# Kernel tuning notes

Measured on AMD Instinct MI355X. Metric: run time of the kernel, lower is better.

Reference implementation:

```python
import jax, jax.numpy as jnp
import numpy as np

HIDDEN = 2048
HEADS = 16
HEAD_DIM = HIDDEN // HEADS
BATCH = 2
SEQ = 2048


def setup_inputs() -> dict:
    key = jax.random.key(0)
    ks = jax.random.split(key, 9)
    s = 0.02
    return {
        "x": jax.random.normal(ks[0], (BATCH, SEQ, HIDDEN), dtype=jnp.float32),
        "Wq": jax.random.normal(ks[1], (HIDDEN, HIDDEN), dtype=jnp.float32) * s,
        "bq": jax.random.normal(ks[2], (HIDDEN,), dtype=jnp.float32) * s,
        "Wk": jax.random.normal(ks[3], (HIDDEN, HIDDEN), dtype=jnp.float32) * s,
        "bk": jax.random.normal(ks[4], (HIDDEN,), dtype=jnp.float32) * s,
        "Wv": jax.random.normal(ks[5], (HIDDEN, HIDDEN), dtype=jnp.float32) * s,
        "bv": jax.random.normal(ks[6], (HIDDEN,), dtype=jnp.float32) * s,
        "Wo": jax.random.normal(ks[7], (HIDDEN, HIDDEN), dtype=jnp.float32) * s,
        "bo": jax.random.normal(ks[8], (HIDDEN,), dtype=jnp.float32) * s,
    }


def reference(x, Wq, bq, Wk, bk, Wv, bv, Wo, bo):
    B, S, H = x.shape
    # Linear layers: y = x @ W.T + b (torch nn.Linear convention, W:[out,in])
    q = x @ Wq.T + bq
    k = x @ Wk.T + bk
    v = x @ Wv.T + bv
    # [B, S, H] -> [B, nH, S, hd]
    def split_heads(t):
        return t.reshape(B, S, HEADS, HEAD_DIM).transpose(0, 2, 1, 3)
    q, k, v = split_heads(q), split_heads(k), split_heads(v)
    scale = 1.0 / (HEAD_DIM ** 0.5)
    # NOTE: original module applies NO causal mask despite its name; be faithful.
    scores = jnp.einsum('bhqd,bhkd->bhqk', q, k) * scale
    probs = jax.nn.softmax(scores, axis=-1)
    attn = jnp.einsum('bhqk,bhkd->bhqd', probs, v)
    attn = attn.transpose(0, 2, 1, 3).reshape(B, S, H)
    return attn @ Wo.T + bo
```

## Files before the change

### kernel.cpp

```cpp
#include <hip/hip_runtime.h>
#include <hip/hip_bf16.h>
#include <stdint.h>

typedef __bf16 bf16_t;
typedef __attribute__((ext_vector_type(8))) __bf16 bf16x8;
typedef __attribute__((ext_vector_type(4))) float floatx4;
typedef __attribute__((ext_vector_type(16))) float f32x16;

typedef __attribute__((address_space(1))) const unsigned int gu32_t;
typedef __attribute__((address_space(3))) unsigned int lu32_t;

#define SL2E 0.12753102149f

__device__ __forceinline__ void async16(const void* g, void* l) {
    __builtin_amdgcn_global_load_lds((gu32_t*)g, (lu32_t*)l, 16, 0, 0);
}

__device__ __forceinline__ uint32_t pack2(float lo, float hi) {
    union { bf16_t h[2]; uint32_t u; } cv;
    cv.h[0] = (bf16_t)lo; cv.h[1] = (bf16_t)hi;
    return cv.u;
}

__global__ __launch_bounds__(256) void cvt_all(const float* __restrict__ x,
                                               const float* __restrict__ w0,
                                               const float* __restrict__ w1,
                                               const float* __restrict__ w2,
                                               const float* __restrict__ w3,
                                               bf16_t* __restrict__ out) {
    int b = blockIdx.x;
    const float* in;
    if (b < 4096) {
        in = x + (size_t)b * 2048;
    } else {
        int t = b - 4096;
        const float* wsrc[4] = {w0, w1, w2, w3};
        in = wsrc[t >> 11] + (size_t)(t & 2047) * 2048;
    }
    bf16_t* o = out + (size_t)b * 2048;
    int i = threadIdx.x * 8;
    float4 a = *(const float4*)(in + i);
    float4 c = *(const float4*)(in + i + 4);
    bf16x8 v;
    v[0] = (bf16_t)a.x; v[1] = (bf16_t)a.y; v[2] = (bf16_t)a.z; v[3] = (bf16_t)a.w;
    v[4] = (bf16_t)c.x; v[5] = (bf16_t)c.y; v[6] = (bf16_t)c.z; v[7] = (bf16_t)c.w;
    *(bf16x8*)(o + i) = v;
}

__global__ __launch_bounds__(256) void gemm_qkv(const bf16_t* __restrict__ xb,
                                                const bf16_t* __restrict__ wqk,
                                                const bf16_t* __restrict__ wv,
                                                const float* __restrict__ bq,
                                                const float* __restrict__ bk,
                                                const float* __restrict__ bv,
                                                bf16_t* __restrict__ QKb,
                                                bf16_t* __restrict__ Vtb) {
    __shared__ bf16_t As[128 * 64];
    __shared__ bf16_t Bs[128 * 64];
    const int tid = threadIdx.x;
    const int wave = tid >> 6, lane = tid & 63;
    const int quad = lane >> 4, l16 = lane & 15;
    const int wm = (wave >> 1) * 64, wn = (wave & 1) * 64;

    const int bid = blockIdx.x;
    const bool vmode = bid >= 1024;
    int tm, tn;
    const bf16_t *A, *B;
    bf16_t* Cb;
    if (!vmode) { tm = (bid & 31) * 128; tn = (bid >> 5) * 128; A = xb; B = wqk; Cb = QKb; }
    else { int vb = bid - 1024; tm = (vb & 15) * 128; tn = (vb >> 4) * 128; A = wv; B = xb; Cb = Vtb; }
    const int K = 2048, ldc = 4096;

    floatx4 acc[4][4];
#pragma unroll
    for (int i = 0; i < 4; ++i)
#pragma unroll
        for (int j = 0; j < 4; ++j) acc[i][j] = floatx4{0.f, 0.f, 0.f, 0.f};

    const bf16_t* Abase = A + (size_t)tm * K;
    const bf16_t* Bbase = B + (size_t)tn * K;
    const int sw = l16 & 7;

    for (int kk = 0; kk < K; kk += 64) {
#pragma unroll
        for (int it = 0; it < 4; ++it) {
            int chunk = it * 256 + tid;
            int r = chunk >> 3, c = chunk & 7;
            int c2 = c ^ (r & 7);
            async16(Abase + r * K + kk + c2 * 8, As + (it * 256 + wave * 64) * 8);
            async16(Bbase + r * K + kk + c2 * 8, Bs + (it * 256 + wave * 64) * 8);
        }
        __syncthreads();
#pragma unroll
        for (int ks = 0; ks < 2; ++ks) {
            bf16x8 af[4], bf[4];
#pragma unroll
            for (int mt = 0; mt < 4; ++mt)
                af[mt] = *(const bf16x8*)(As + (wm + mt * 16 + l16) * 64 +
                                          ((ks * 4 + quad) ^ sw) * 8);
#pragma unroll
            for (int nt = 0; nt < 4; ++nt)
                bf[nt] = *(const bf16x8*)(Bs + (wn + nt * 16 + l16) * 64 +
                                          ((ks * 4 + quad) ^ sw) * 8);
#pragma unroll
            for (int mt = 0; mt < 4; ++mt)
#pragma unroll
                for (int nt = 0; nt < 4; ++nt)
                    acc[mt][nt] = __builtin_amdgcn_mfma_f32_16x16x32_bf16(af[mt], bf[nt],
                                                                          acc[mt][nt], 0, 0, 0);
        }
        __syncthreads();
    }
#pragma unroll
    for (int mt = 0; mt < 4; ++mt)
#pragma unroll
        for (int nt = 0; nt < 4; ++nt)
#pragma unroll
            for (int r = 0; r < 4; ++r) {
                int row = tm + wm + mt * 16 + quad * 4 + r;
                int col = tn + wn + nt * 16 + l16;
                float v;
                if (vmode) v = acc[mt][nt][r] + bv[row];
                else if (col < 2048) v = (acc[mt][nt][r] + bq[col]) * SL2E;
                else v = acc[mt][nt][r] + bk[col - 2048];
                Cb[(size_t)row * ldc + col] = (bf16_t)v;
            }
}

__global__ __launch_bounds__(256) void gemm_out(const bf16_t* __restrict__ A,
                                                const bf16_t* __restrict__ B,
                                                const float* __restrict__ bias,
                                                float* __restrict__ Cf,
                                                int K, int ldc) {
    __shared__ bf16_t As[128 * 64];
    __shared__ bf16_t Bs[128 * 64];
    const int tid = threadIdx.x;
    const int wave = tid >> 6, lane = tid & 63;
    const int quad = lane >> 4, l16 = lane & 15;
    const int wm = (wave >> 1) * 64, wn = (wave & 1) * 64;
    const int tm = blockIdx.x * 128, tn = blockIdx.y * 128;

    floatx4 acc[4][4];
#pragma unroll
    for (int i = 0; i < 4; ++i)
#pragma unroll
        for (int j = 0; j < 4; ++j) acc[i][j] = floatx4{0.f, 0.f, 0.f, 0.f};

    const bf16_t* Abase = A + (size_t)tm * K;
    const bf16_t* Bbase = B + (size_t)tn * K;
    const int sw = l16 & 7;

    for (int kk = 0; kk < K; kk += 64) {
#pragma unroll
        for (int it = 0; it < 4; ++it) {
            int chunk = it * 256 + tid;
            int r = chunk >> 3, c = chunk & 7;
            int c2 = c ^ (r & 7);
            async16(Abase + r * K + kk + c2 * 8, As + (it * 256 + wave * 64) * 8);
            async16(Bbase + r * K + kk + c2 * 8, Bs + (it * 256 + wave * 64) * 8);
        }
        __syncthreads();
#pragma unroll
        for (int ks = 0; ks < 2; ++ks) {
            bf16x8 af[4], bf[4];
#pragma unroll
            for (int mt = 0; mt < 4; ++mt)
                af[mt] = *(const bf16x8*)(As + (wm + mt * 16 + l16) * 64 +
                                          ((ks * 4 + quad) ^ sw) * 8);
#pragma unroll
            for (int nt = 0; nt < 4; ++nt)
                bf[nt] = *(const bf16x8*)(Bs + (wn + nt * 16 + l16) * 64 +
                                          ((ks * 4 + quad) ^ sw) * 8);
#pragma unroll
            for (int mt = 0; mt < 4; ++mt)
#pragma unroll
                for (int nt = 0; nt < 4; ++nt)
                    acc[mt][nt] = __builtin_amdgcn_mfma_f32_16x16x32_bf16(af[mt], bf[nt],
                                                                          acc[mt][nt], 0, 0, 0);
        }
        __syncthreads();
    }
#pragma unroll
    for (int mt = 0; mt < 4; ++mt)
#pragma unroll
        for (int nt = 0; nt < 4; ++nt)
#pragma unroll
            for (int r = 0; r < 4; ++r) {
                int row = tm + wm + mt * 16 + quad * 4 + r;
                int col = tn + wn + nt * 16 + l16;
                Cf[(size_t)row * ldc + col] = acc[mt][nt][r] + bias[col];
            }
}

#define FA_BUF (64 * 128 + 128 * 64)
__global__ __launch_bounds__(256, 2) void flash_attn(const bf16_t* __restrict__ Qp,
                                                     const bf16_t* __restrict__ Kp,
                                                     const bf16_t* __restrict__ Vt,
                                                     bf16_t* __restrict__ O) {
    __shared__ bf16_t smem[2 * FA_BUF];
    const int tid = threadIdx.x;
    const int wv = tid >> 6, lane = tid & 63;
    const int hi = lane >> 5, l32 = lane & 31;
    const int wq = wv >> 1, wk = wv & 1;
    const int LD = 4096, T = 4096, S = 2048, HO = 2048;

    const int gid = blockIdx.x;
    const int kq = gid >> 3;
    const int qt = kq & 15;
    const int grp = (gid & 7) + 8 * (kq >> 4);
    const int hd = grp & 15, bt = grp >> 4;

    const int qrow0 = bt * S + qt * 128;
    const int krow0 = bt * S;
    const int hoff = hd * 128;
    const int sw7 = l32 & 7;

    bf16x8 qf[2][8];
#pragma unroll
    for (int g = 0; g < 2; ++g) {
        const bf16_t* qptr = Qp + (size_t)(qrow0 + wq * 64 + g * 32 + l32) * LD + hoff + hi * 8;
#pragma unroll
        for (int ks = 0; ks < 8; ++ks) qf[g][ks] = *(const bf16x8*)(qptr + ks * 16);
    }

    float l_i[2] = {0.f, 0.f};
    f32x16 Oacc[2][4];
#pragma unroll
    for (int g = 0; g < 2; ++g)
#pragma unroll
        for (int dt = 0; dt < 4; ++dt)
#pragma unroll
            for (int r = 0; r < 16; ++r) Oacc[g][dt][r] = 0.f;

    auto stage = [&](int kt, int b) {
        int kb = krow0 + kt * 64;
        bf16_t* Ks = smem + b * FA_BUF;
        bf16_t* Vts = Ks + 64 * 128;
#pragma unroll
        for (int it = 0; it < 4; ++it) {
            int chunk = it * 256 + tid;
            int r = chunk >> 4, c = chunk & 15;
            int c2 = c ^ (r & 7);
            async16(Kp + (size_t)(kb + r) * LD + hoff + c2 * 8, Ks + chunk * 8);
        }
#pragma unroll
        for (int it = 0; it < 4; ++it) {
            int chunk = it * 256 + tid;
            int r = chunk >> 3, c = chunk & 7;
            int c2 = c ^ (r & 7);
            async16(Vt + (size_t)(hoff + r) * T + kb + c2 * 8, Vts + chunk * 8);
        }
    };

    stage(0, 0);
    for (int kt = 0; kt < 32; ++kt) {
        const int cur = kt & 1;
        __syncthreads();
        if (kt + 1 < 32) stage(kt + 1, cur ^ 1);

        const bf16_t* Ks = smem + cur * FA_BUF;
        const bf16_t* Vts = Ks + 64 * 128;

        uint32_t pk[2][8];
#pragma unroll
        for (int g = 0; g < 2; ++g) {
            f32x16 sf;
#pragma unroll
            for (int r = 0; r < 16; ++r) sf[r] = 0.f;
#pragma unroll
            for (int ks = 0; ks < 8; ++ks) {
                bf16x8 a = *(const bf16x8*)(Ks + (wk * 32 + l32) * 128 +
                                            ((2 * ks + hi) ^ sw7) * 8);
                sf = __builtin_amdgcn_mfma_f32_32x32x16_bf16(a, qf[g][ks], sf, 0, 0, 0);
            }
            float rs0 = 0.f, rs1 = 0.f;
#pragma unroll
            for (int a4 = 0; a4 < 4; ++a4) {
                float p0 = exp2f(sf[4 * a4 + 0]);
                float p1 = exp2f(sf[4 * a4 + 1]);
                float p2 = exp2f(sf[4 * a4 + 2]);
                float p3 = exp2f(sf[4 * a4 + 3]);
                rs0 += p0 + p1;
                rs1 += p2 + p3;
                pk[g][a4 * 2 + 0] = pack2(p0, p1);
                pk[g][a4 * 2 + 1] = pack2(p2, p3);
            }
            l_i[g] += rs0 + rs1;
        }

#pragma unroll
        for (int s = 0; s < 2; ++s) {
            union { uint32_t u[4]; bf16x8 v; } w[2];
#pragma unroll
            for (int g = 0; g < 2; ++g) {
                uint32_t r0 = (uint32_t)__shfl_xor((int)pk[g][4 * s + 0], 32);
                uint32_t r1 = (uint32_t)__shfl_xor((int)pk[g][4 * s + 1], 32);
                uint32_t r2 = (uint32_t)__shfl_xor((int)pk[g][4 * s + 2], 32);
                uint32_t r3 = (uint32_t)__shfl_xor((int)pk[g][4 * s + 3], 32);
                w[g].u[0] = hi ? r2 : pk[g][4 * s + 0];
                w[g].u[1] = hi ? r3 : pk[g][4 * s + 1];
                w[g].u[2] = hi ? pk[g][4 * s + 2] : r0;
                w[g].u[3] = hi ? pk[g][4 * s + 3] : r1;
            }
#pragma unroll
            for (int dt = 0; dt < 4; ++dt) {
                bf16x8 av = *(const bf16x8*)(Vts + (dt * 32 + l32) * 64 +
                                             ((4 * wk + 2 * s + hi) ^ sw7) * 8);
                Oacc[0][dt] = __builtin_amdgcn_mfma_f32_32x32x16_bf16(av, w[0].v, Oacc[0][dt], 0, 0, 0);
                Oacc[1][dt] = __builtin_amdgcn_mfma_f32_32x32x16_bf16(av, w[1].v, Oacc[1][dt], 0, 0, 0);
            }
        }
    }

    __syncthreads();
    float* ml = (float*)smem;
#pragma unroll
    for (int g = 0; g < 2; ++g) l_i[g] += __shfl_xor(l_i[g], 32);
    if (hi == 0) {
        ml[(wv * 2 + 0) * 32 + l32] = l_i[0];
        ml[(wv * 2 + 1) * 32 + l32] = l_i[1];
    }
    __syncthreads();
    float linv[2];
#pragma unroll
    for (int g = 0; g < 2; ++g)
        linv[g] = 1.0f / (l_i[g] + ml[((wv ^ 1) * 2 + g) * 32 + l32]);
    __syncthreads();

    float* Op = (float*)smem;
    if (wk == 1) {
#pragma unroll
        for (int g = 0; g < 2; ++g)
#pragma unroll
            for (int dt = 0; dt < 4; ++dt)
#pragma unroll
                for (int r = 0; r < 16; ++r) {
                    int d = dt * 32 + (r & 3) + 8 * (r >> 2) + 4 * hi;
                    Op[((wq * 2 + g) * 128 + d) * 32 + l32] = Oacc[g][dt][r];
                }
    }
    __syncthreads();
    if (wk == 0) {
#pragma unroll
        for (int g = 0; g < 2; ++g)
#pragma unroll
            for (int dt = 0; dt < 4; ++dt)
#pragma unroll
                for (int r = 0; r < 16; ++r) {
                    int d = dt * 32 + (r & 3) + 8 * (r >> 2) + 4 * hi;
                    Oacc[g][dt][r] = (Oacc[g][dt][r] +
                                      Op[((wq * 2 + g) * 128 + d) * 32 + l32]) * linv[g];
                }
    }
    __syncthreads();

    if (wk == 0) {
        uint32_t* Os = (uint32_t*)smem + wq * 4096;
#pragma unroll
        for (int g = 0; g < 2; ++g)
#pragma unroll
            for (int dt = 0; dt < 4; ++dt)
#pragma unroll
                for (int a4 = 0; a4 < 4; ++a4) {
                    uint32_t q0 = pack2(Oacc[g][dt][4 * a4 + 0], Oacc[g][dt][4 * a4 + 1]);
                    uint32_t q1 = pack2(Oacc[g][dt][4 * a4 + 2], Oacc[g][dt][4 * a4 + 3]);
                    int d2 = 16 * dt + 4 * a4 + 2 * hi;
                    int row = g * 32 + l32;
                    Os[row * 64 + ((d2 + 2 * l32) & 63)] = q0;
                    Os[row * 64 + ((d2 + 1 + 2 * l32) & 63)] = q1;
                }
    }
    __syncthreads();
#pragma unroll
    for (int r2 = 0; r2 < 32; ++r2) {
        int rr = wv * 32 + r2;
        int wqs = rr >> 6, r = rr & 63;
        uint32_t v = ((uint32_t*)smem)[wqs * 4096 + r * 64 + ((lane + 2 * r) & 63)];
        uint32_t* orow = (uint32_t*)(O + (size_t)(qrow0 + wqs * 64 + r) * HO + hoff);
        orow[lane] = v;
    }
}

extern "C" void kernel_launch(void* const* d_in, const int* in_sizes, int n_in,
                              void* d_out, int out_size, void* d_ws, size_t ws_size,
                              hipStream_t stream) {
    const float* x  = (const float*)d_in[0];
    const float* Wq = (const float*)d_in[1];
    const float* bq = (const float*)d_in[2];
    const float* Wk = (const float*)d_in[3];
    const float* bk = (const float*)d_in[4];
    const float* Wv = (const float*)d_in[5];
    const float* bv = (const float*)d_in[6];
    const float* Wo = (const float*)d_in[7];
    const float* bo = (const float*)d_in[8];
    float* out = (float*)d_out;

    const int T = 4096;
    const int H = 2048;
    bf16_t* ws  = (bf16_t*)d_ws;
    bf16_t* xb  = ws;
    bf16_t* wqb = xb  + (size_t)T * H;
    bf16_t* wvb = wqb + 2 * (size_t)H * H;
    bf16_t* wob = wvb + (size_t)H * H;
    bf16_t* QKb = wob + (size_t)H * H;
    bf16_t* Vtb = QKb + (size_t)T * 2 * H;
    bf16_t* Ab  = Vtb + (size_t)H * T;
    size_t need = (size_t)(Ab + (size_t)T * H - ws) * sizeof(bf16_t);
    if (ws_size < need) return;

    cvt_all<<<12288, 256, 0, stream>>>(x, Wq, Wk, Wv, Wo, ws);

    gemm_qkv<<<1536, 256, 0, stream>>>(xb, wqb, wvb, bq, bk, bv, QKb, Vtb);

    flash_attn<<<512, 256, 0, stream>>>(QKb, QKb + H, Vtb, Ab);

    dim3 go(T / 128, H / 128);
    gemm_out<<<go, 256, 0, stream>>>(Ab, wob, bo, out, H, H);
}
```

Before: 456.7 us.

## Double-buffer GEMM LDS tiles and halve flash-attention query tile per block

Both GEMM kernels now keep two LDS buffers and issue the async global-to-LDS loads for the next K slice before computing on the current one. This removes one barrier per iteration and is meant to overlap memory traffic with MFMA work. LDS use doubles to 64KB per block, with launch bounds of two blocks per CU. The flash-attention kernel now handles 64 query rows per block instead of 128, launched over 1024 blocks, which cuts register pressure and adds parallelism but reloads K/V tiles twice as often.

```diff
diff --git a/kernel.cpp b/kernel.cpp
--- a/kernel.cpp
+++ b/kernel.cpp
@@ -47,16 +47,16 @@
     *(bf16x8*)(o + i) = v;
 }
 
-__global__ __launch_bounds__(256) void gemm_qkv(const bf16_t* __restrict__ xb,
-                                                const bf16_t* __restrict__ wqk,
-                                                const bf16_t* __restrict__ wv,
-                                                const float* __restrict__ bq,
-                                                const float* __restrict__ bk,
-                                                const float* __restrict__ bv,
-                                                bf16_t* __restrict__ QKb,
-                                                bf16_t* __restrict__ Vtb) {
-    __shared__ bf16_t As[128 * 64];
-    __shared__ bf16_t Bs[128 * 64];
+#define GB (128 * 64)
+__global__ __launch_bounds__(256, 2) void gemm_qkv(const bf16_t* __restrict__ xb,
+                                                   const bf16_t* __restrict__ wqk,
+                                                   const bf16_t* __restrict__ wv,
+                                                   const float* __restrict__ bq,
+                                                   const float* __restrict__ bk,
+                                                   const float* __restrict__ bv,
+                                                   bf16_t* __restrict__ QKb,
+                                                   bf16_t* __restrict__ Vtb) {
+    __shared__ bf16_t smem[4 * GB];
     const int tid = threadIdx.x;
     const int wave = tid >> 6, lane = tid & 63;
     const int quad = lane >> 4, l16 = lane & 15;
@@ -81,7 +81,9 @@
     const bf16_t* Bbase = B + (size_t)tn * K;
     const int sw = l16 & 7;
 
-    for (int kk = 0; kk < K; kk += 64) {
+    auto stageAB = [&](int kk, int b) {
+        bf16_t* As = smem + b * 2 * GB;
+        bf16_t* Bs = As + GB;
 #pragma unroll
         for (int it = 0; it < 4; ++it) {
             int chunk = it * 256 + tid;
@@ -90,7 +92,15 @@
             async16(Abase + r * K + kk + c2 * 8, As + (it * 256 + wave * 64) * 8);
             async16(Bbase + r * K + kk + c2 * 8, Bs + (it * 256 + wave * 64) * 8);
         }
+    };
+
+    stageAB(0, 0);
+    for (int ki = 0; ki < 32; ++ki) {
+        const int cur = ki & 1;
         __syncthreads();
+        if (ki + 1 < 32) stageAB((ki + 1) * 64, cur ^ 1);
+        const bf16_t* As = smem + cur * 2 * GB;
+        const bf16_t* Bs = As + GB;
 #pragma unroll
         for (int ks = 0; ks < 2; ++ks) {
             bf16x8 af[4], bf[4];
@@ -109,7 +119,6 @@
                     acc[mt][nt] = __builtin_amdgcn_mfma_f32_16x16x32_bf16(af[mt], bf[nt],
                                                                           acc[mt][nt], 0, 0, 0);
         }
-        __syncthreads();
     }
 #pragma unroll
     for (int mt = 0; mt < 4; ++mt)
@@ -127,13 +136,12 @@
             }
 }
 
-__global__ __launch_bounds__(256) void gemm_out(const bf16_t* __restrict__ A,
-                                                const bf16_t* __restrict__ B,
-                                                const float* __restrict__ bias,
-                                                float* __restrict__ Cf,
-                                                int K, int ldc) {
-    __shared__ bf16_t As[128 * 64];
-    __shared__ bf16_t Bs[128 * 64];
+__global__ __launch_bounds__(256, 2) void gemm_out(const bf16_t* __restrict__ A,
+                                                   const bf16_t* __restrict__ B,
+                                                   const float* __restrict__ bias,
+                                                   float* __restrict__ Cf,
+                                                   int K, int ldc) {
+    __shared__ bf16_t smem[4 * GB];
     const int tid = threadIdx.x;
     const int wave = tid >> 6, lane = tid & 63;
     const int quad = lane >> 4, l16 = lane & 15;
@@ -149,8 +157,11 @@
     const bf16_t* Abase = A + (size_t)tm * K;
     const bf16_t* Bbase = B + (size_t)tn * K;
     const int sw = l16 & 7;
-
-    for (int kk = 0; kk < K; kk += 64) {
+    const int nIter = K / 64;
+
+    auto stageAB = [&](int kk, int b) {
+        bf16_t* As = smem + b * 2 * GB;
+        bf16_t* Bs = As + GB;
 #pragma unroll
         for (int it = 0; it < 4; ++it) {
             int chunk = it * 256 + tid;
@@ -159,7 +170,15 @@
             async16(Abase + r * K + kk + c2 * 8, As + (it * 256 + wave * 64) * 8);
             async16(Bbase + r * K + kk + c2 * 8, Bs + (it * 256 + wave * 64) * 8);
         }
+    };
+
+    stageAB(0, 0);
+    for (int ki = 0; ki < nIter; ++ki) {
+        const int cur = ki & 1;
         __syncthreads();
+        if (ki + 1 < nIter) stageAB((ki + 1) * 64, cur ^ 1);
+        const bf16_t* As = smem + cur * 2 * GB;
+        const bf16_t* Bs = As + GB;
 #pragma unroll
         for (int ks = 0; ks < 2; ++ks) {
             bf16x8 af[4], bf[4];
@@ -178,7 +197,6 @@
                     acc[mt][nt] = __builtin_amdgcn_mfma_f32_16x16x32_bf16(af[mt], bf[nt],
                                                                           acc[mt][nt], 0, 0, 0);
         }
-        __syncthreads();
     }
 #pragma unroll
     for (int mt = 0; mt < 4; ++mt)
@@ -206,31 +224,26 @@
 
     const int gid = blockIdx.x;
     const int kq = gid >> 3;
-    const int qt = kq & 15;
-    const int grp = (gid & 7) + 8 * (kq >> 4);
+    const int qt = kq & 31;
+    const int grp = (gid & 7) + 8 * (kq >> 5);
     const int hd = grp & 15, bt = grp >> 4;
 
-    const int qrow0 = bt * S + qt * 128;
+    const int qrow0 = bt * S + qt * 64;
     const int krow0 = bt * S;
     const int hoff = hd * 128;
     const int sw7 = l32 & 7;
 
-    bf16x8 qf[2][8];
-#pragma unroll
-    for (int g = 0; g < 2; ++g) {
-        const bf16_t* qptr = Qp + (size_t)(qrow0 + wq * 64 + g * 32 + l32) * LD + hoff + hi * 8;
-#pragma unroll
-        for (int ks = 0; ks < 8; ++ks) qf[g][ks] = *(const bf16x8*)(qptr + ks * 16);
-    }
-
-    float l_i[2] = {0.f, 0.f};
-    f32x16 Oacc[2][4];
-#pragma unroll
-    for (int g = 0; g < 2; ++g)
-#pragma unroll
-        for (int dt = 0; dt < 4; ++dt)
-#pragma unroll
-            for (int r = 0; r < 16; ++r) Oacc[g][dt][r] = 0.f;
+    bf16x8 qf[8];
+    const bf16_t* qptr = Qp + (size_t)(qrow0 + wq * 32 + l32) * LD + hoff + hi * 8;
+#pragma unroll
+    for (int ks = 0; ks < 8; ++ks) qf[ks] = *(const bf16x8*)(qptr + ks * 16);
+
+    float l_i = 0.f;
+    f32x16 Oacc[4];
+#pragma unroll
+    for (int dt = 0; dt < 4; ++dt)
+#pragma unroll
+        for (int r = 0; r < 16; ++r) Oacc[dt][r] = 0.f;
 
     auto stage = [&](int kt, int b) {
         int kb = krow0 + kt * 64;
@@ -261,123 +274,102 @@
         const bf16_t* Ks = smem + cur * FA_BUF;
         const bf16_t* Vts = Ks + 64 * 128;
 
-        uint32_t pk[2][8];
-#pragma unroll
-        for (int g = 0; g < 2; ++g) {
-            f32x16 sf;
-#pragma unroll
-            for (int r = 0; r < 16; ++r) sf[r] = 0.f;
-#pragma unroll
-            for (int ks = 0; ks < 8; ++ks) {
-                bf16x8 a = *(const bf16x8*)(Ks + (wk * 32 + l32) * 128 +
-                                            ((2 * ks + hi) ^ sw7) * 8);
-                sf = __builtin_amdgcn_mfma_f32_32x32x16_bf16(a, qf[g][ks], sf, 0, 0, 0);
-            }
-            float rs0 = 0.f, rs1 = 0.f;
-#pragma unroll
-            for (int a4 = 0; a4 < 4; ++a4) {
-                float p0 = exp2f(sf[4 * a4 + 0]);
-                float p1 = exp2f(sf[4 * a4 + 1]);
-                float p2 = exp2f(sf[4 * a4 + 2]);
-                float p3 = exp2f(sf[4 * a4 + 3]);
-                rs0 += p0 + p1;
-                rs1 += p2 + p3;
-                pk[g][a4 * 2 + 0] = pack2(p0, p1);
-                pk[g][a4 * 2 + 1] = pack2(p2, p3);
-            }
-            l_i[g] += rs0 + rs1;
-        }
+        f32x16 sf0, sf1;
+#pragma unroll
+        for (int r = 0; r < 16; ++r) { sf0[r] = 0.f; sf1[r] = 0.f; }
+#pragma unroll
+        for (int ks = 0; ks < 4; ++ks) {
+            bf16x8 a0 = *(const bf16x8*)(Ks + (wk * 32 + l32) * 128 +
+                                         ((2 * ks + hi) ^ sw7) * 8);
+            bf16x8 a1 = *(const bf16x8*)(Ks + (wk * 32 + l32) * 128 +
+                                         ((2 * (ks + 4) + hi) ^ sw7) * 8);
+            sf0 = __builtin_amdgcn_mfma_f32_32x32x16_bf16(a0, qf[ks], sf0, 0, 0, 0);
+            sf1 = __builtin_amdgcn_mfma_f32_32x32x16_bf16(a1, qf[ks + 4], sf1, 0, 0, 0);
+        }
+
+        float rs0 = 0.f, rs1 = 0.f;
+        uint32_t pk[8];
+#pragma unroll
+        for (int a4 = 0; a4 < 4; ++a4) {
+            float p0 = exp2f(sf0[4 * a4 + 0] + sf1[4 * a4 + 0]);
+            float p1 = exp2f(sf0[4 * a4 + 1] + sf1[4 * a4 + 1]);
+            float p2 = exp2f(sf0[4 * a4 + 2] + sf1[4 * a4 + 2]);
+            float p3 = exp2f(sf0[4 * a4 + 3] + sf1[4 * a4 + 3]);
+            rs0 += p0 + p1;
+            rs1 += p2 + p3;
+            pk[a4 * 2 + 0] = pack2(p0, p1);
+            pk[a4 * 2 + 1] = pack2(p2, p3);
+        }
+        l_i += rs0 + rs1;
 
 #pragma unroll
         for (int s = 0; s < 2; ++s) {
-            union { uint32_t u[4]; bf16x8 v; } w[2];
-#pragma unroll
-            for (int g = 0; g < 2; ++g) {
-                uint32_t r0 = (uint32_t)__shfl_xor((int)pk[g][4 * s + 0], 32);
-                uint32_t r1 = (uint32_t)__shfl_xor((int)pk[g][4 * s + 1], 32);
-                uint32_t r2 = (uint32_t)__shfl_xor((int)pk[g][4 * s + 2], 32);
-                uint32_t r3 = (uint32_t)__shfl_xor((int)pk[g][4 * s + 3], 32);
-                w[g].u[0] = hi ? r2 : pk[g][4 * s + 0];
-                w[g].u[1] = hi ? r3 : pk[g][4 * s + 1];
-                w[g].u[2] = hi ? pk[g][4 * s + 2] : r0;
-                w[g].u[3] = hi ? pk[g][4 * s + 3] : r1;
-            }
+            uint32_t r0 = (uint32_t)__shfl_xor((int)pk[4 * s + 0], 32);
+            uint32_t r1 = (uint32_t)__shfl_xor((int)pk[4 * s + 1], 32);
+            uint32_t r2 = (uint32_t)__shfl_xor((int)pk[4 * s + 2], 32);
+            uint32_t r3 = (uint32_t)__shfl_xor((int)pk[4 * s + 3], 32);
+            union { uint32_t u[4]; bf16x8 v; } w;
+            w.u[0] = hi ? r2 : pk[4 * s + 0];
+            w.u[1] = hi ? r3 : pk[4 * s + 1];
+            w.u[2] = hi ? pk[4 * s + 2] : r0;
+            w.u[3] = hi ? pk[4 * s + 3] : r1;
 #pragma unroll
             for (int dt = 0; dt < 4; ++dt) {
-                bf16x8 av = *(const bf16x8*)(Vts + (dt * 32 + l32) * 64 +
-                                             ((4 * wk + 2 * s + hi) ^ sw7) * 8);
-                Oacc[0][dt] = __builtin_amdgcn_mfma_f32_32x32x16_bf16(av, w[0].v, Oacc[0][dt], 0, 0, 0);
-                Oacc[1][dt] = __builtin_amdgcn_mfma_f32_32x32x16_bf16(av, w[1].v, Oacc[1][dt], 0, 0, 0);
+                bf16x8 a = *(const bf16x8*)(Vts + (dt * 32 + l32) * 64 +
+                                            ((4 * wk + 2 * s + hi) ^ sw7) * 8);
+                Oacc[dt] = __builtin_amdgcn_mfma_f32_32x32x16_bf16(a, w.v, Oacc[dt], 0, 0, 0);
             }
         }
     }
 
     __syncthreads();
+    l_i += __shfl_xor(l_i, 32);
     float* ml = (float*)smem;
-#pragma unroll
-    for (int g = 0; g < 2; ++g) l_i[g] += __shfl_xor(l_i[g], 32);
-    if (hi == 0) {
-        ml[(wv * 2 + 0) * 32 + l32] = l_i[0];
-        ml[(wv * 2 + 1) * 32 + l32] = l_i[1];
-    }
+    if (hi == 0) ml[wv * 32 + l32] = l_i;
     __syncthreads();
-    float linv[2];
-#pragma unroll
-    for (int g = 0; g < 2; ++g)
-        linv[g] = 1.0f / (l_i[g] + ml[((wv ^ 1) * 2 + g) * 32 + l32]);
+    float linv = 1.0f / (l_i + ml[(wv ^ 1) * 32 + l32]);
     __syncthreads();
 
     float* Op = (float*)smem;
     if (wk == 1) {
 #pragma unroll
-        for (int g = 0; g < 2; ++g)
-#pragma unroll
-            for (int dt = 0; dt < 4; ++dt)
-#pragma unroll
-                for (int r = 0; r < 16; ++r) {
-                    int d = dt * 32 + (r & 3) + 8 * (r >> 2) + 4 * hi;
-                    Op[((wq * 2 + g) * 128 + d) * 32 + l32] = Oacc[g][dt][r];
-                }
+        for (int dt = 0; dt < 4; ++dt)
+#pragma unroll
+            for (int r = 0; r < 16; ++r) {
+                int d = dt * 32 + (r & 3) + 8 * (r >> 2) + 4 * hi;
+                Op[(wq * 128 + d) * 32 + l32] = Oacc[dt][r];
+            }
     }
     __syncthreads();
     if (wk == 0) {
 #pragma unroll
-        for (int g = 0; g < 2; ++g)
-#pragma unroll
-            for (int dt = 0; dt < 4; ++dt)
-#pragma unroll
-                for (int r = 0; r < 16; ++r) {
-                    int d = dt * 32 + (r & 3) + 8 * (r >> 2) + 4 * hi;
-                    Oacc[g][dt][r] = (Oacc[g][dt][r] +
-                                      Op[((wq * 2 + g) * 128 + d) * 32 + l32]) * linv[g];
-                }
+        for (int dt = 0; dt < 4; ++dt)
+#pragma unroll
+            for (int r = 0; r < 16; ++r) {
+                int d = dt * 32 + (r & 3) + 8 * (r >> 2) + 4 * hi;
+                Oacc[dt][r] = (Oacc[dt][r] + Op[(wq * 128 + d) * 32 + l32]) * linv;
+            }
     }
     __syncthreads();
 
     if (wk == 0) {
-        uint32_t* Os = (uint32_t*)smem + wq * 4096;
-#pragma unroll
-        for (int g = 0; g < 2; ++g)
-#pragma unroll
-            for (int dt = 0; dt < 4; ++dt)
-#pragma unroll
-                for (int a4 = 0; a4 < 4; ++a4) {
-                    uint32_t q0 = pack2(Oacc[g][dt][4 * a4 + 0], Oacc[g][dt][4 * a4 + 1]);
-                    uint32_t q1 = pack2(Oacc[g][dt][4 * a4 + 2], Oacc[g][dt][4 * a4 + 3]);
-                    int d2 = 16 * dt + 4 * a4 + 2 * hi;
-                    int row = g * 32 + l32;
-                    Os[row * 64 + ((d2 + 2 * l32) & 63)] = q0;
-                    Os[row * 64 + ((d2 + 1 + 2 * l32) & 63)] = q1;
-                }
-    }
-    __syncthreads();
-#pragma unroll
-    for (int r2 = 0; r2 < 32; ++r2) {
-        int rr = wv * 32 + r2;
-        int wqs = rr >> 6, r = rr & 63;
-        uint32_t v = ((uint32_t*)smem)[wqs * 4096 + r * 64 + ((lane + 2 * r) & 63)];
-        uint32_t* orow = (uint32_t*)(O + (size_t)(qrow0 + wqs * 64 + r) * HO + hoff);
-        orow[lane] = v;
+        uint32_t* Os = (uint32_t*)smem + wq * 2048;
+#pragma unroll
+        for (int dt = 0; dt < 4; ++dt)
+#pragma unroll
+            for (int a4 = 0; a4 < 4; ++a4) {
+                uint32_t q0 = pack2(Oacc[dt][4 * a4 + 0], Oacc[dt][4 * a4 + 1]);
+                uint32_t q1 = pack2(Oacc[dt][4 * a4 + 2], Oacc[dt][4 * a4 + 3]);
+                int d2 = 16 * dt + 4 * a4 + 2 * hi;
+                Os[l32 * 64 + ((d2 + 2 * l32) & 63)] = q0;
+                Os[l32 * 64 + ((d2 + 1 + 2 * l32) & 63)] = q1;
+            }
+#pragma unroll
+        for (int r = 0; r < 32; ++r) {
+            uint32_t v = Os[r * 64 + ((lane + 2 * r) & 63)];
+            uint32_t* orow = (uint32_t*)(O + (size_t)(qrow0 + wq * 32 + r) * HO + hoff);
+            orow[lane] = v;
+        }
     }
 }
 
@@ -412,7 +404,7 @@
 
     gemm_qkv<<<1536, 256, 0, stream>>>(xb, wqb, wvb, bq, bk, bv, QKb, Vtb);
 
-    flash_attn<<<512, 256, 0, stream>>>(QKb, QKb + H, Vtb, Ab);
+    flash_attn<<<1024, 256, 0, stream>>>(QKb, QKb + H, Vtb, Ab);
 
     dim3 go(T / 128, H / 128);
     gemm_out<<<go, 256, 0, stream>>>(Ab, wob, bo, out, H, H);
```

Result: faster. 428.6 us (-6.2%).
